# Optimization experiments

Measured on AMD Instinct MI355X. Metric: run time of the kernel, lower is better.

The kernel has to match this reference:

```python
import jax, jax.numpy as jnp
import numpy as np

H = 2048; HQ = 16; HKV = 4; G = HQ // HKV; D = 128; S = 2048
KS = 32; KSTRIDE = 16; BS = 128; TOPK = 8
INIT_BLK = 1; LOCAL_BLK = 2; WIN = 512
THETA = 500000.0
N_CMP = (S - KS) // KSTRIDE + 1
N_BLK = S // BS
NEG = -1e30


def _rope_inv_freq():
    # llama3-style frequency scaling (factor 8, high 4, low 1, orig 8192)
    inv = 1.0 / (THETA ** (np.arange(0, D, 2, dtype=np.float64) / D))
    factor, lo_f, hi_f, orig = 8.0, 1.0, 4.0, 8192.0
    wav = 2.0 * np.pi / inv
    smooth = (orig / wav - lo_f) / (hi_f - lo_f)
    inv_s = np.where(wav > orig / lo_f, inv / factor,
                     np.where(wav < orig / hi_f, inv,
                              (1.0 - smooth) * inv / factor + smooth * inv))
    return jnp.asarray(inv_s, dtype=jnp.float32)


def _rope(x):
    # x: [S, h, D]
    ang = jnp.arange(x.shape[0], dtype=jnp.float32)[:, None] * _rope_inv_freq()[None, :]
    cos = jnp.cos(ang)[:, None, :]
    sin = jnp.sin(ang)[:, None, :]
    x1, x2 = x[..., : D // 2], x[..., D // 2:]
    return jnp.concatenate([x1 * cos - x2 * sin, x2 * cos + x1 * sin], axis=-1)


def setup_inputs() -> dict:
    key = jax.random.key(0)
    ks = jax.random.split(key, 8)
    std = 0.02
    return {
        'hidden_states': jax.random.normal(ks[0], (1, S, H), jnp.float32),
        'Wq': jax.random.normal(ks[1], (H, HQ * D), jnp.float32) * std,
        'Wk': jax.random.normal(ks[2], (H, HKV * D), jnp.float32) * std,
        'Wv': jax.random.normal(ks[3], (H, HKV * D), jnp.float32) * std,
        'Wo': jax.random.normal(ks[4], (HQ * D, H), jnp.float32) * std,
        'Wg': jax.random.normal(ks[5], (H, HQ * 3), jnp.float32) * std,
        'Wck': jax.random.normal(ks[6], (HKV, KS * D, D), jnp.float32) * std,
        'Wcv': jax.random.normal(ks[7], (HKV, KS * D, D), jnp.float32) * std,
    }


def _nsa_forward(hidden_states, Wq, Wk, Wv, Wo, Wg, Wck, Wcv):
    x = hidden_states[0]                                  # [S, H] (bsz=1, packed)
    q = _rope((x @ Wq).reshape(S, HQ, D))                 # [S, HQ, D]
    k = _rope((x @ Wk).reshape(S, HKV, D))                # [S, HKV, D]
    v = (x @ Wv).reshape(S, HKV, D)
    scale = D ** -0.5
    pos = jnp.arange(S)
    qg = q.reshape(S, HKV, G, D)

    # ---- branch 1: compressed attention (overlapping windows, learned pooling) ----
    starts = jnp.arange(N_CMP) * KSTRIDE
    widx = starts[:, None] + jnp.arange(KS)[None, :]      # [N_CMP, KS]
    kw = k[widx].transpose(2, 0, 1, 3).reshape(HKV, N_CMP, KS * D)
    vw = v[widx].transpose(2, 0, 1, 3).reshape(HKV, N_CMP, KS * D)
    ck = jnp.einsum('hnf,hfd->hnd', kw, Wck)              # [HKV, N_CMP, D]
    cv = jnp.einsum('hnf,hfd->hnd', vw, Wcv)
    s_cmp = jnp.einsum('shgd,hnd->hgsn', qg, ck) * scale  # [HKV, G, S, N_CMP]
    m_cmp = (starts + KS)[None, :] <= pos[:, None] + 1    # fully-past compressed blocks
    has_cmp = m_cmp.any(axis=-1).astype(s_cmp.dtype)      # [S]
    p_cmp = jax.nn.softmax(jnp.where(m_cmp[None, None], s_cmp, NEG), axis=-1)
    p_cmp = p_cmp * has_cmp[None, None, :, None]
    o_cmp = jnp.einsum('hgsn,hnd->shgd', p_cmp, cv).reshape(S, HQ, D)

    # ---- branch 2: top-k block-selected attention ----
    cmp2blk = (starts // BS)[:, None] == jnp.arange(N_BLK)[None, :]
    bscore = jnp.einsum('hgsn,nb->hsb', p_cmp, cmp2blk.astype(p_cmp.dtype))  # GQA-group sum
    qblk = pos // BS
    blks = jnp.arange(N_BLK)
    forced = (blks[None, :] < INIT_BLK) | ((blks[None, :] <= qblk[:, None]) & (blks[None, :] > qblk[:, None] - LOCAL_BLK))
    _, top_idx = jax.lax.top_k(bscore + forced[None].astype(bscore.dtype) * 1e9, TOPK)
    sel_blk = jnp.any(top_idx[..., None] == blks, axis=-2)  # [HKV, S, N_BLK]

    causal = pos[None, :] <= pos[:, None]                    # [S, S]
    raw = jnp.einsum('shgd,nhd->hgsn', qg, k) * scale        # [HKV, G, S, S] (shared by branches 2/3)

    m_sel = jnp.repeat(sel_blk, BS, axis=-1) & causal[None]  # [HKV, S, S]
    p_sel = jax.nn.softmax(jnp.where(m_sel[:, None], raw, NEG), axis=-1)
    o_sel = jnp.einsum('hgsn,nhd->shgd', p_sel, v).reshape(S, HQ, D)

    # ---- branch 3: sliding-window attention ----
    m_win = causal & (pos[None, :] > pos[:, None] - WIN)
    p_win = jax.nn.softmax(jnp.where(m_win[None, None], raw, NEG), axis=-1)
    o_win = jnp.einsum('hgsn,nhd->shgd', p_win, v).reshape(S, HQ, D)

    # ---- per-head sigmoid gates mixing the three branches ----
    g = jax.nn.sigmoid(x @ Wg).reshape(S, HQ, 3)
    o = g[..., 0:1] * o_cmp + g[..., 1:2] * o_sel + g[..., 2:3] * o_win
    return (o.reshape(S, HQ * D) @ Wo)[None]                 # [1, S, H]


def reference(hidden_states, Wq, Wk, Wv, Wo, Wg, Wck, Wcv):
    return _nsa_forward(hidden_states, Wq, Wk, Wv, Wo, Wg, Wck, Wcv)
```

## Files before the change

kernel.cpp:

```cpp
#include <hip/hip_runtime.h>
#include <math.h>

#define SS 2048
#define HH 2048
#define HQ 16
#define HKV 4
#define GG 4
#define DD 128
#define KS 32
#define KSTRIDE 16
#define NCMP 127
#define NBLK 16
#define TOPK 8
#define WINSZ 512
#define TQ 16

typedef unsigned short u16;
typedef __bf16 bf16x8 __attribute__((ext_vector_type(8)));
typedef __bf16 bf16x4 __attribute__((ext_vector_type(4)));
typedef float f32x4 __attribute__((ext_vector_type(4)));

__device__ __forceinline__ u16 f2bf(float f) {
    __bf16 b = (__bf16)f;
    return __builtin_bit_cast(u16, b);
}

__device__ __forceinline__ int xcd_swz(int id, int nwg) {
    if (nwg & 7) return id;
    int cpx = nwg >> 3;
    return (id & 7) * cpx + (id >> 3);
}

__global__ void rope_tab(float* __restrict__ cost, float* __restrict__ sint) {
    int s = blockIdx.x;
    int i = threadIdx.x;
    double inv = pow(500000.0, -(double)i / 64.0);
    double wav = 6.283185307179586476925286766559 / inv;
    double inv_s;
    if (wav > 8192.0) inv_s = inv / 8.0;
    else if (wav < 2048.0) inv_s = inv;
    else {
        double sm = (8192.0 / wav - 1.0) / 3.0;
        inv_s = (1.0 - sm) * inv / 8.0 + sm * inv;
    }
    float ang = (float)s * (float)inv_s;
    cost[s * 64 + i] = cosf(ang);
    sint[s * 64 + i] = sinf(ang);
}

__global__ void rope_bf16(const float* __restrict__ src, u16* __restrict__ dst,
                          const float* __restrict__ cost, const float* __restrict__ sint,
                          int nh, float scale) {
    int s = blockIdx.x, h = blockIdx.y, i = threadIdx.x;
    const float* p = src + ((size_t)s * nh + h) * DD;
    float c = cost[s * 64 + i], sn = sint[s * 64 + i];
    float x1 = p[i], x2 = p[i + 64];
    u16* d = dst + ((size_t)s * nh + h) * DD;
    d[i] = f2bf((x1 * c - x2 * sn) * scale);
    d[i + 64] = f2bf((x2 * c + x1 * sn) * scale);
}

__global__ void sigmoid_k(float* __restrict__ x, int n) {
    int i = blockIdx.x * 256 + threadIdx.x;
    if (i < n) x[i] = 1.f / (1.f + __expf(-x[i]));
}

__global__ void conv_bf16(const float* __restrict__ in, u16* __restrict__ out, int n4) {
    int i = blockIdx.x * 256 + threadIdx.x;
    if (i < n4) {
        float4 v = ((const float4*)in)[i];
        ushort4 o;
        o.x = f2bf(v.x); o.y = f2bf(v.y); o.z = f2bf(v.z); o.w = f2bf(v.w);
        ((ushort4*)out)[i] = o;
    }
}

__global__ __launch_bounds__(256) void conv_vt(const float* __restrict__ v, u16* __restrict__ vt) {
    __shared__ float tile[32][33];
    int s0 = blockIdx.x * 32, d0 = blockIdx.y * 32, h = blockIdx.z;
    int tx = threadIdx.x & 31, ty = threadIdx.x >> 5;
#pragma unroll
    for (int i = 0; i < 32; i += 8)
        tile[ty + i][tx] = v[(size_t)(s0 + ty + i) * (HKV * DD) + h * DD + d0 + tx];
    __syncthreads();
#pragma unroll
    for (int i = 0; i < 32; i += 8)
        vt[(size_t)h * DD * SS + (size_t)(d0 + ty + i) * SS + s0 + tx] = f2bf(tile[tx][ty + i]);
}

__global__ __launch_bounds__(256) void convT(const float* __restrict__ W, u16* __restrict__ Bt,
                                             int K, int N, int Npad,
                                             size_t wz, size_t bz) {
    __shared__ float tile[32][33];
    W += (size_t)blockIdx.z * wz;
    Bt += (size_t)blockIdx.z * bz;
    int bk = blockIdx.x * 32, bn = blockIdx.y * 32;
    int tx = threadIdx.x & 31, ty = threadIdx.x >> 5;
#pragma unroll
    for (int i = 0; i < 32; i += 8) {
        int k = bk + ty + i, n = bn + tx;
        tile[ty + i][tx] = (n < N) ? W[(size_t)k * N + n] : 0.f;
    }
    __syncthreads();
#pragma unroll
    for (int i = 0; i < 32; i += 8) {
        int n = bn + ty + i, k = bk + tx;
        if (n < Npad) Bt[(size_t)n * K + k] = f2bf(tile[tx][ty + i]);
    }
}

__device__ __forceinline__ void gload16(const void* g, void* l) {
    __builtin_amdgcn_global_load_lds((const __attribute__((address_space(1))) void*)g,
                                     (__attribute__((address_space(3))) void*)l, 16, 0, 0);
}

__global__ __launch_bounds__(256) void gemm_mfma(const u16* __restrict__ A,
                                                 const u16* __restrict__ Bt,
                                                 float* __restrict__ C,
                                                 int M, int N, int K) {
    __shared__ __align__(16) u16 Asm[128 * 64];
    __shared__ __align__(16) u16 Bsm[128 * 64];
    int t = threadIdx.x;
    int lane = t & 63;
    int w = t >> 6;
    int wm = w >> 1, wn = w & 1;
    int nwg = gridDim.x * gridDim.y;
    int id = xcd_swz(blockIdx.y * gridDim.x + blockIdx.x, nwg);
    int bxs = id % gridDim.x, bys = id / gridDim.x;
    int bm = bys * 128, bn = bxs * 128;
    int lr = lane & 15, hi = lane >> 4;

    f32x4 acc[4][4] = {};
    for (int k0 = 0; k0 < K; k0 += 64) {
        if (k0) __syncthreads();
#pragma unroll
        for (int i = 0; i < 4; ++i) {
            int cflat = i * 256 + t;
            int m = cflat >> 3;
            int g = cflat & 7;
            int gl = g ^ (m & 7);
            unsigned lofs = (unsigned)((i * 256 + (t & ~63)) * 16);
            gload16(A + (size_t)(bm + m) * K + k0 + gl * 8, (char*)Asm + lofs);
            gload16(Bt + (size_t)(bn + m) * K + k0 + gl * 8, (char*)Bsm + lofs);
        }
        __syncthreads();
#pragma unroll
        for (int kk = 0; kk < 2; ++kk) {
            bf16x8 af[4], bf[4];
#pragma unroll
            for (int mi = 0; mi < 4; ++mi) {
                int row = wm * 64 + mi * 16 + lr;
                int g = (kk * 4 + hi) ^ (row & 7);
                af[mi] = *reinterpret_cast<const bf16x8*>(&Asm[row * 64 + g * 8]);
            }
#pragma unroll
            for (int ni = 0; ni < 4; ++ni) {
                int row = wn * 64 + ni * 16 + lr;
                int g = (kk * 4 + hi) ^ (row & 7);
                bf[ni] = *reinterpret_cast<const bf16x8*>(&Bsm[row * 64 + g * 8]);
            }
#pragma unroll
            for (int mi = 0; mi < 4; ++mi)
#pragma unroll
                for (int ni = 0; ni < 4; ++ni)
                    acc[mi][ni] = __builtin_amdgcn_mfma_f32_16x16x32_bf16(af[mi], bf[ni], acc[mi][ni], 0, 0, 0);
        }
    }
#pragma unroll
    for (int mi = 0; mi < 4; ++mi) {
#pragma unroll
        for (int ni = 0; ni < 4; ++ni) {
            int col = bn + wn * 64 + ni * 16 + lr;
            if (col < N) {
#pragma unroll
                for (int r = 0; r < 4; ++r) {
                    int row = bm + wm * 64 + mi * 16 + hi * 4 + r;
                    C[(size_t)row * N + col] = acc[mi][ni][r];
                }
            }
        }
    }
}

__global__ __launch_bounds__(256) void gemm_proj(const u16* __restrict__ A,
                                                 const u16* __restrict__ BtQ,
                                                 const u16* __restrict__ BtK,
                                                 const u16* __restrict__ BtV,
                                                 const u16* __restrict__ BtG,
                                                 float* __restrict__ Cq,
                                                 float* __restrict__ Ck,
                                                 float* __restrict__ Cv,
                                                 float* __restrict__ Cg) {
    __shared__ __align__(16) u16 Asm[128 * 64];
    __shared__ __align__(16) u16 Bsm[128 * 64];
    int nwg = gridDim.x * gridDim.y;
    int id = xcd_swz(blockIdx.y * gridDim.x + blockIdx.x, nwg);
    int bx = id % gridDim.x, by = id / gridDim.x;
    const u16* Bt; float* C; int N; int bn;
    if (bx < 16)      { Bt = BtQ; C = Cq; N = 2048; bn = bx * 128; }
    else if (bx < 20) { Bt = BtK; C = Ck; N = 512;  bn = (bx - 16) * 128; }
    else if (bx < 24) { Bt = BtV; C = Cv; N = 512;  bn = (bx - 20) * 128; }
    else              { Bt = BtG; C = Cg; N = 48;   bn = 0; }
    const int K = 2048;
    int t = threadIdx.x, lane = t & 63, w = t >> 6;
    int wm = w >> 1, wn = w & 1;
    int bm = by * 128;
    int lr = lane & 15, hi = lane >> 4;

    f32x4 acc[4][4] = {};
    for (int k0 = 0; k0 < K; k0 += 64) {
        if (k0) __syncthreads();
#pragma unroll
        for (int i = 0; i < 4; ++i) {
            int cflat = i * 256 + t;
            int m = cflat >> 3;
            int g = cflat & 7;
            int gl = g ^ (m & 7);
            unsigned lofs = (unsigned)((i * 256 + (t & ~63)) * 16);
            gload16(A + (size_t)(bm + m) * K + k0 + gl * 8, (char*)Asm + lofs);
            gload16(Bt + (size_t)(bn + m) * K + k0 + gl * 8, (char*)Bsm + lofs);
        }
        __syncthreads();
#pragma unroll
        for (int kk = 0; kk < 2; ++kk) {
            bf16x8 af[4], bf[4];
#pragma unroll
            for (int mi = 0; mi < 4; ++mi) {
                int row = wm * 64 + mi * 16 + lr;
                int g = (kk * 4 + hi) ^ (row & 7);
                af[mi] = *reinterpret_cast<const bf16x8*>(&Asm[row * 64 + g * 8]);
            }
#pragma unroll
            for (int ni = 0; ni < 4; ++ni) {
                int row = wn * 64 + ni * 16 + lr;
                int g = (kk * 4 + hi) ^ (row & 7);
                bf[ni] = *reinterpret_cast<const bf16x8*>(&Bsm[row * 64 + g * 8]);
            }
#pragma unroll
            for (int mi = 0; mi < 4; ++mi)
#pragma unroll
                for (int ni = 0; ni < 4; ++ni)
                    acc[mi][ni] = __builtin_amdgcn_mfma_f32_16x16x32_bf16(af[mi], bf[ni], acc[mi][ni], 0, 0, 0);
        }
    }
#pragma unroll
    for (int mi = 0; mi < 4; ++mi) {
#pragma unroll
        for (int ni = 0; ni < 4; ++ni) {
            int col = bn + wn * 64 + ni * 16 + lr;
            if (col < N) {
#pragma unroll
                for (int r = 0; r < 4; ++r) {
                    int row = bm + wm * 64 + mi * 16 + hi * 4 + r;
                    C[(size_t)row * N + col] = acc[mi][ni][r];
                }
            }
        }
    }
}

__global__ __launch_bounds__(256) void cmp_kv_split(const u16* __restrict__ Ak,
                                                    const u16* __restrict__ Wkt,
                                                    const u16* __restrict__ Av,
                                                    const u16* __restrict__ Wvt,
                                                    float* __restrict__ partials) {
    __shared__ __align__(16) u16 Asm[128 * 64];
    __shared__ __align__(16) u16 Bsm[128 * 64];
    int z = blockIdx.y, split = blockIdx.x;
    int h = z & 3;
    const u16* A  = (z >> 2) ? Av : Ak;
    const u16* Wt = (z >> 2) ? Wvt : Wkt;
    int t = threadIdx.x, lane = t & 63, w = t >> 6;
    int wm = w >> 1, wn = w & 1;
    int lr = lane & 15, hi = lane >> 4;
    const u16* Wh = Wt + (size_t)h * DD * (KS * DD);

    f32x4 acc[4][4] = {};
    int kbase = split * 256;
    for (int it = 0; it < 4; ++it) {
        int k0 = kbase + it * 64;
        if (it) __syncthreads();
        int roff = k0 >> 7;
        int dbase = ((k0 >> 6) & 1) * 64;
#pragma unroll
        for (int i = 0; i < 4; ++i) {
            int cflat = i * 256 + t;
            int m = cflat >> 3;
            int g = cflat & 7;
            int gl = g ^ (m & 7);
            unsigned lofs = (unsigned)((i * 256 + (t & ~63)) * 16);
            int nr = (m < NCMP) ? m : (NCMP - 1);
            gload16(A + ((size_t)(nr * KSTRIDE + roff) * HKV + h) * DD + dbase + gl * 8,
                    (char*)Asm + lofs);
            gload16(Wh + (size_t)m * (KS * DD) + k0 + gl * 8, (char*)Bsm + lofs);
        }
        __syncthreads();
#pragma unroll
        for (int kk = 0; kk < 2; ++kk) {
            bf16x8 af[4], bf[4];
#pragma unroll
            for (int mi = 0; mi < 4; ++mi) {
                int row = wm * 64 + mi * 16 + lr;
                int g = (kk * 4 + hi) ^ (row & 7);
                af[mi] = *reinterpret_cast<const bf16x8*>(&Asm[row * 64 + g * 8]);
            }
#pragma unroll
            for (int ni = 0; ni < 4; ++ni) {
                int row = wn * 64 + ni * 16 + lr;
                int g = (kk * 4 + hi) ^ (row & 7);
                bf[ni] = *reinterpret_cast<const bf16x8*>(&Bsm[row * 64 + g * 8]);
            }
#pragma unroll
            for (int mi = 0; mi < 4; ++mi)
#pragma unroll
                for (int ni = 0; ni < 4; ++ni)
                    acc[mi][ni] = __builtin_amdgcn_mfma_f32_16x16x32_bf16(af[mi], bf[ni], acc[mi][ni], 0, 0, 0);
        }
    }
    float* Cout = partials + ((size_t)(z * 16 + split)) * 128 * 128;
#pragma unroll
    for (int mi = 0; mi < 4; ++mi)
#pragma unroll
        for (int ni = 0; ni < 4; ++ni) {
            int col = wn * 64 + ni * 16 + lr;
#pragma unroll
            for (int r = 0; r < 4; ++r) {
                int row = wm * 64 + mi * 16 + hi * 4 + r;
                Cout[(size_t)row * 128 + col] = acc[mi][ni][r];
            }
        }
}

__global__ void cmp_kv_reduce(const float* __restrict__ partials,
                              u16* __restrict__ ckbf, u16* __restrict__ cvtbf) {
    int row = blockIdx.x, z = blockIdx.y, col = threadIdx.x;
    float s = 0.f;
#pragma unroll
    for (int sp = 0; sp < 16; ++sp)
        s += partials[(((size_t)z * 16 + sp) * 128 + row) * 128 + col];
    if (z < 4) ckbf[((size_t)z * 128 + row) * 128 + col] = f2bf(s);
    else       cvtbf[((size_t)(z - 4) * 128 + col) * 128 + row] = f2bf(s);
}

__global__ __launch_bounds__(256) void cmp_attn_mfma(
    const u16* __restrict__ qbf,
    const u16* __restrict__ ckbf,
    const u16* __restrict__ cvtbf,
    const float* __restrict__ gate,
    float* __restrict__ o_acc,
    unsigned int* __restrict__ sel) {
    __shared__ __align__(16) u16 Cks[128 * 128];
    __shared__ __align__(16) u16 P2[4][16 * 128];
    __shared__ float bs[4][16][16];
    int t = threadIdx.x, lane = t & 63, w = t >> 6;
    int lr = lane & 15, hi = lane >> 4;
    int s0 = blockIdx.x * 16, h = blockIdx.y;
    int hq = h * GG + w;
    int sr = s0 + lr;
    const u16* ckh = ckbf + (size_t)h * 128 * 128;
    const u16* cvh = cvtbf + (size_t)h * 128 * 128;
    bf16x8 qf[4];
#pragma unroll
    for (int ks = 0; ks < 4; ++ks)
        qf[ks] = *reinterpret_cast<const bf16x8*>(
            &qbf[((size_t)sr * HQ + hq) * DD + ks * 32 + hi * 8]);
#pragma unroll
    for (int i = 0; i < 8; ++i) {
        int id = i * 256 + t;
        int key = id >> 4, sub = id & 15;
        gload16(ckh + (size_t)key * 128 + ((sub ^ (key & 7)) * 8),
                (char*)Cks + (id & ~63) * 16);
    }
    __syncthreads();
    f32x4 sacc[8] = {};
#pragma unroll
    for (int ks = 0; ks < 4; ++ks)
#pragma unroll
        for (int mt = 0; mt < 8; ++mt) {
            int row = mt * 16 + lr;
            bf16x8 kf = *reinterpret_cast<const bf16x8*>(
                &Cks[row * 128 + (((ks * 4 + hi) ^ (row & 7)) * 8)]);
            sacc[mt] = __builtin_amdgcn_mfma_f32_16x16x32_bf16(kf, qf[ks], sacc[mt], 0, 0, 0);
        }
    int nv = (sr >= 31) ? ((sr - 31) >> 4) + 1 : 0;
    float e[8][4];
    float mx = -1e30f;
#pragma unroll
    for (int mt = 0; mt < 8; ++mt)
#pragma unroll
        for (int r = 0; r < 4; ++r) {
            int n = mt * 16 + hi * 4 + r;
            float x = (n < nv) ? sacc[mt][r] : -1e30f;
            e[mt][r] = x;
            mx = fmaxf(mx, x);
        }
    mx = fmaxf(mx, __shfl_xor(mx, 16, 64));
    mx = fmaxf(mx, __shfl_xor(mx, 32, 64));
    float l = 0.f;
#pragma unroll
    for (int mt = 0; mt < 8; ++mt)
#pragma unroll
        for (int r = 0; r < 4; ++r) {
            int n = mt * 16 + hi * 4 + r;
            float p = (n < nv) ? __expf(e[mt][r] - mx) : 0.f;
            e[mt][r] = p;
            l += p;
        }
    l += __shfl_xor(l, 16, 64);
    l += __shfl_xor(l, 32, 64);
    float invl = (nv > 0) ? 1.f / l : 0.f;
#pragma unroll
    for (int mt = 0; mt < 8; ++mt)
#pragma unroll
        for (int r = 0; r < 4; ++r) e[mt][r] *= invl;
#pragma unroll
    for (int mt = 0; mt < 8; ++mt) {
        bf16x4 pk;
        pk[0] = (__bf16)e[mt][0]; pk[1] = (__bf16)e[mt][1];
        pk[2] = (__bf16)e[mt][2]; pk[3] = (__bf16)e[mt][3];
        int grp = mt * 2 + (hi >> 1);
        int idx = lr * 128 + ((grp ^ (lr & 7)) * 8) + (hi & 1) * 4;
        *reinterpret_cast<bf16x4*>(&P2[w][idx]) = pk;
    }
#pragma unroll
    for (int mt = 0; mt < 8; ++mt) {
        float s4 = e[mt][0] + e[mt][1] + e[mt][2] + e[mt][3];
        float v = s4 + __shfl_xor(s4, 16, 64);
        if (hi == 0) bs[w][lr][mt * 2] = v;
        else if (hi == 2) bs[w][lr][mt * 2 + 1] = v;
    }
    __syncthreads();
    bf16x8 pa[4];
#pragma unroll
    for (int kslot = 0; kslot < 4; ++kslot)
        pa[kslot] = *reinterpret_cast<const bf16x8*>(
            &P2[w][lr * 128 + (((kslot * 4 + hi) ^ (lr & 7)) * 8)]);
    f32x4 Os[8] = {};
#pragma unroll
    for (int nt = 0; nt < 8; ++nt) {
        int d = nt * 16 + lr;
#pragma unroll
        for (int kslot = 0; kslot < 4; ++kslot) {
            bf16x8 bv = *reinterpret_cast<const bf16x8*>(
                &cvh[(size_t)d * 128 + kslot * 32 + hi * 8]);
            Os[nt] = __builtin_amdgcn_mfma_f32_16x16x32_bf16(pa[kslot], bv, Os[nt], 0, 0, 0);
        }
    }
#pragma unroll
    for (int r = 0; r < 4; ++r) {
        int q = hi * 4 + r;
        int srow = s0 + q;
        float g0 = gate[((size_t)srow * HQ + hq) * 3 + 0];
#pragma unroll
        for (int nt = 0; nt < 8; ++nt) {
            size_t idx = ((size_t)srow * HQ + hq) * DD + nt * 16 + lr;
            o_acc[idx] = g0 * Os[nt][r];
        }
    }
    if (t < 16) {
        int q = t, s = s0 + q;
        int qblk = s >> 7;
#pragma unroll
        for (int b = 0; b < 16; ++b) {
            bool forced = (b == 0) || (b <= qblk && b > qblk - 2);
            bs[0][q][b] = bs[0][q][b] + bs[1][q][b] + bs[2][q][b] + bs[3][q][b]
                          + (forced ? 1e9f : 0.f);
        }
        unsigned int mask = 0;
        for (int it = 0; it < TOPK; ++it) {
            int arg = 0; float best = bs[0][q][0];
            for (int b = 1; b < 16; ++b) {
                float x = bs[0][q][b];
                if (x > best) { best = x; arg = b; }
            }
            mask |= 1u << arg;
            bs[0][q][arg] = -1e38f;
        }
        sel[s * HKV + h] = mask;
    }
}

__global__ __launch_bounds__(256, 3) void sel_win_mfma(
    const u16* __restrict__ qbf,
    const u16* __restrict__ kbf,
    const u16* __restrict__ vtbf,
    const float* __restrict__ gate,
    const unsigned int* __restrict__ sel,
    const float* __restrict__ oacc,
    u16* __restrict__ outb) {
    __shared__ __align__(16) u16 Ks[64 * 128];
    __shared__ __align__(16) u16 Vs[128 * 64];
    __shared__ __align__(16) u16 P2[4][2][16 * 64];
    __shared__ unsigned int sml[16];
    int t = threadIdx.x, lane = t & 63, w = t >> 6;
    int lr = lane & 15, hi = lane >> 4;
    int s0 = (gridDim.x - 1 - blockIdx.x) * 16;
    int h = blockIdx.y;
    int hq = h * GG + w;
    int sr = s0 + lr;
    if (t < 16) sml[t] = sel[(s0 + t) * HKV + h];
    bf16x8 qf[4];
#pragma unroll
    for (int ks = 0; ks < 4; ++ks)
        qf[ks] = *reinterpret_cast<const bf16x8*>(
            &qbf[((size_t)(s0 + lr) * HQ + hq) * DD + ks * 32 + hi * 8]);
    __syncthreads();
    unsigned mymask = sml[lr];
    unsigned orMask = 0;
#pragma unroll
    for (int i = 0; i < 16; ++i) orMask |= sml[i];
    float m_u = -1e30f, l_s = 0.f, l_w = 0.f;
    f32x4 Os[8] = {}, Ow[8] = {};
    int smax = s0 + 15;
    const u16* vbase = vtbf + (size_t)h * DD * SS;

    for (int kb = 0; kb * 128 <= smax; ++kb) {
        bool needSel = (orMask >> kb) & 1u;
        bool selbit = needSel && ((mymask >> kb) & 1u);
        for (int half = 0; half < 2; ++half) {
            int hst = kb * 128 + half * 64;
            if (hst > smax) break;
            bool hWin = (hst + 63 >= s0 - (WINSZ - 1));
            if (!(needSel || hWin)) continue;
            __syncthreads();
#pragma unroll
            for (int i = 0; i < 4; ++i) {
                int id = i * 256 + t;
                int key = id >> 4, dq = id & 15;
                gload16(kbf + ((size_t)(hst + key) * HKV + h) * DD + ((dq ^ (key & 7)) * 8),
                        (char*)Ks + (id & ~63) * 16);
                int d = id >> 3, kq = id & 7;
                gload16(vbase + (size_t)d * SS + hst + ((kq ^ (d & 7)) * 8),
                        (char*)Vs + (id & ~63) * 16);
            }
            __syncthreads();
            f32x4 sacc[4] = {};
            __builtin_amdgcn_s_setprio(1);
#pragma unroll
            for (int ks = 0; ks < 4; ++ks) {
#pragma unroll
                for (int mt = 0; mt < 4; ++mt) {
                    int key = mt * 16 + lr;
                    bf16x8 kf = *reinterpret_cast<const bf16x8*>(
                        &Ks[key * 128 + (((ks * 4 + hi) ^ (key & 7)) * 8)]);
                    sacc[mt] = __builtin_amdgcn_mfma_f32_16x16x32_bf16(kf, qf[ks], sacc[mt], 0, 0, 0);
                }
            }
            __builtin_amdgcn_s_setprio(0);
            float e4[4][4];
            float mx = -1e30f;
#pragma unroll
            for (int mt = 0; mt < 4; ++mt)
#pragma unroll
                for (int r = 0; r < 4; ++r) {
                    int key = hst + mt * 16 + hi * 4 + r;
                    bool vS = selbit && (key <= sr);
                    bool vW = hWin && (key <= sr) && (key > sr - WINSZ);
                    float e = (vS || vW) ? sacc[mt][r] : -1e30f;
                    e4[mt][r] = e;
                    mx = fmaxf(mx, e);
                }
            mx = fmaxf(mx, __shfl_xor(mx, 16, 64));
            mx = fmaxf(mx, __shfl_xor(mx, 32, 64));
            if (!__all(mx - m_u <= 8.f)) {
                float newm = fmaxf(m_u, mx);
                float corr = __expf(m_u - newm);
                m_u = newm;
                l_s *= corr; l_w *= corr;
#pragma unroll
                for (int r = 0; r < 4; ++r) {
                    float c2 = __shfl(corr, hi * 4 + r, 64);
#pragma unroll
                    for (int nt = 0; nt < 8; ++nt) { Os[nt][r] *= c2; Ow[nt][r] *= c2; }
                }
            }
            float lsA = 0.f, lwA = 0.f;
#pragma unroll
            for (int mt = 0; mt < 4; ++mt)
#pragma unroll
                for (int r = 0; r < 4; ++r) {
                    int key = hst + mt * 16 + hi * 4 + r;
                    bool vS = selbit && (key <= sr);
                    bool vW = hWin && (key <= sr) && (key > sr - WINSZ);
                    float e = (vS || vW) ? __expf(e4[mt][r] - m_u) : 0.f;
                    e4[mt][r] = e;
                    lsA += vS ? e : 0.f;
                    lwA += vW ? e : 0.f;
                }
            lsA += __shfl_xor(lsA, 16, 64); lsA += __shfl_xor(lsA, 32, 64);
            lwA += __shfl_xor(lwA, 16, 64); lwA += __shfl_xor(lwA, 32, 64);
            l_s += lsA; l_w += lwA;
            if (needSel) {
#pragma unroll
                for (int mt = 0; mt < 4; ++mt) {
                    bf16x4 pk;
#pragma unroll
                    for (int r = 0; r < 4; ++r) {
                        int key = hst + mt * 16 + hi * 4 + r;
                        bool vS = selbit && (key <= sr);
                        pk[r] = (__bf16)(vS ? e4[mt][r] : 0.f);
                    }
                    int grp = mt * 2 + (hi >> 1);
                    int idx = lr * 64 + ((grp ^ (lr & 7)) * 8) + (hi & 1) * 4;
                    *reinterpret_cast<bf16x4*>(&P2[w][0][idx]) = pk;
                }
            }
            if (hWin) {
#pragma unroll
                for (int mt = 0; mt < 4; ++mt) {
                    bf16x4 pk;
#pragma unroll
                    for (int r = 0; r < 4; ++r) {
                        int key = hst + mt * 16 + hi * 4 + r;
                        bool vW = (key <= sr) && (key > sr - WINSZ);
                        pk[r] = (__bf16)(vW ? e4[mt][r] : 0.f);
                    }
                    int grp = mt * 2 + (hi >> 1);
                    int idx = lr * 64 + ((grp ^ (lr & 7)) * 8) + (hi & 1) * 4;
                    *reinterpret_cast<bf16x4*>(&P2[w][1][idx]) = pk;
                }
            }
            bf16x8 pas0, pas1, paw0, paw1;
            if (needSel) {
                pas0 = *reinterpret_cast<const bf16x8*>(&P2[w][0][lr * 64 + (((0 + hi) ^ (lr & 7)) * 8)]);
                pas1 = *reinterpret_cast<const bf16x8*>(&P2[w][0][lr * 64 + (((4 + hi) ^ (lr & 7)) * 8)]);
            }
            if (hWin) {
                paw0 = *reinterpret_cast<const bf16x8*>(&P2[w][1][lr * 64 + (((0 + hi) ^ (lr & 7)) * 8)]);
                paw1 = *reinterpret_cast<const bf16x8*>(&P2[w][1][lr * 64 + (((4 + hi) ^ (lr & 7)) * 8)]);
            }
            __builtin_amdgcn_s_setprio(1);
#pragma unroll
            for (int nt = 0; nt < 8; ++nt) {
                int d = nt * 16 + lr;
                bf16x8 bv0 = *reinterpret_cast<const bf16x8*>(&Vs[d * 64 + (((0 + hi) ^ (d & 7)) * 8)]);
                bf16x8 bv1 = *reinterpret_cast<const bf16x8*>(&Vs[d * 64 + (((4 + hi) ^ (d & 7)) * 8)]);
                if (needSel) {
                    Os[nt] = __builtin_amdgcn_mfma_f32_16x16x32_bf16(pas0, bv0, Os[nt], 0, 0, 0);
                    Os[nt] = __builtin_amdgcn_mfma_f32_16x16x32_bf16(pas1, bv1, Os[nt], 0, 0, 0);
                }
                if (hWin) {
                    Ow[nt] = __builtin_amdgcn_mfma_f32_16x16x32_bf16(paw0, bv0, Ow[nt], 0, 0, 0);
                    Ow[nt] = __builtin_amdgcn_mfma_f32_16x16x32_bf16(paw1, bv1, Ow[nt], 0, 0, 0);
                }
            }
            __builtin_amdgcn_s_setprio(0);
        }
    }
    float invls = (l_s > 0.f) ? 1.f / l_s : 0.f;
    float invlw = (l_w > 0.f) ? 1.f / l_w : 0.f;
#pragma unroll
    for (int r = 0; r < 4; ++r) {
        int q = hi * 4 + r;
        int srow = s0 + q;
        float a1 = gate[((size_t)srow * HQ + hq) * 3 + 1] * __shfl(invls, q, 64);
        float a2 = gate[((size_t)srow * HQ + hq) * 3 + 2] * __shfl(invlw, q, 64);
#pragma unroll
        for (int nt = 0; nt < 8; ++nt) {
            size_t idx = ((size_t)srow * HQ + hq) * DD + nt * 16 + lr;
            outb[idx] = f2bf(oacc[idx] + a1 * Os[nt][r] + a2 * Ow[nt][r]);
        }
    }
}

extern "C" void kernel_launch(void* const* d_in, const int* in_sizes, int n_in,
                              void* d_out, int out_size, void* d_ws, size_t ws_size,
                              hipStream_t stream) {
    const float* x   = (const float*)d_in[0];
    const float* Wq  = (const float*)d_in[1];
    const float* Wk  = (const float*)d_in[2];
    const float* Wv  = (const float*)d_in[3];
    const float* Wo  = (const float*)d_in[4];
    const float* Wg  = (const float*)d_in[5];
    const float* Wck = (const float*)d_in[6];
    const float* Wcv = (const float*)d_in[7];
    float* out = (float*)d_out;
    char* w = (char*)d_ws;
    float* qb   = (float*)(w + 0);
    float* kb   = (float*)(w + 16777216);
    float* vb   = (float*)(w + 20971520);
    float* g3   = (float*)(w + 25165824);
    u16* ckbf   = (u16*)(w + 25559040);
    u16* cvtbf  = (u16*)(w + 25819136);
    unsigned int* selb = (unsigned int*)(w + 26079232);
    float* cost = (float*)(w + 26112000);
    float* sint = (float*)(w + 26636288);
    float* oacc = (float*)(w + 27160576);
    u16* xb     = (u16*)(w + 43937792);
    u16* oaccb  = (u16*)(w + 52326400);
    u16* Wq_t   = (u16*)(w + 60715008);
    u16* Wo_t   = (u16*)(w + 69103616);
    u16* Wk_t   = (u16*)(w + 77492224);
    u16* Wv_t   = (u16*)(w + 79589376);
    u16* Wg_t   = (u16*)(w + 81686528);
    u16* qbf = Wq_t;
    u16* kbf = Wk_t;
    u16* vtbf = Wv_t;
    u16* vbf = (u16*)kb;
    u16* Wck_t = oaccb;
    u16* Wcv_t = xb;
    float* partials = oacc;

    hipLaunchKernelGGL(rope_tab, dim3(SS), dim3(64), 0, stream, cost, sint);
    hipLaunchKernelGGL(conv_bf16, dim3(4096), dim3(256), 0, stream, x, xb, SS * HH / 4);
    hipLaunchKernelGGL(convT, dim3(64, 64), dim3(256), 0, stream, Wq, Wq_t, HH, 2048, 2048, 0, 0);
    hipLaunchKernelGGL(convT, dim3(64, 16), dim3(256), 0, stream, Wk, Wk_t, HH, 512, 512, 0, 0);
    hipLaunchKernelGGL(convT, dim3(64, 16), dim3(256), 0, stream, Wv, Wv_t, HH, 512, 512, 0, 0);
    hipLaunchKernelGGL(convT, dim3(64, 4),  dim3(256), 0, stream, Wg, Wg_t, HH, 48, 128, 0, 0);
    hipLaunchKernelGGL(convT, dim3(64, 64), dim3(256), 0, stream, Wo, Wo_t, HQ * DD, 2048, 2048, 0, 0);
    hipLaunchKernelGGL(gemm_proj, dim3(25, 16), dim3(256), 0, stream,
                       xb, Wq_t, Wk_t, Wv_t, Wg_t, qb, kb, vb, g3);
    hipLaunchKernelGGL(rope_bf16, dim3(SS, HQ),  dim3(64), 0, stream, qb, qbf, cost, sint, HQ, 0.08838834764831845f);
    hipLaunchKernelGGL(rope_bf16, dim3(SS, HKV), dim3(64), 0, stream, kb, kbf, cost, sint, HKV, 1.0f);
    hipLaunchKernelGGL(sigmoid_k, dim3((SS * HQ * 3 + 255) / 256), dim3(256), 0, stream, g3, SS * HQ * 3);
    hipLaunchKernelGGL(conv_bf16, dim3(1024), dim3(256), 0, stream, vb, vbf, SS * HKV * DD / 4);
    hipLaunchKernelGGL(conv_vt, dim3(64, 4, 4), dim3(256), 0, stream, vb, vtbf);
    hipLaunchKernelGGL(convT, dim3(128, 4, 4), dim3(256), 0, stream,
                       Wck, Wck_t, KS * DD, DD, DD, (size_t)KS * DD * DD, (size_t)DD * KS * DD);
    hipLaunchKernelGGL(convT, dim3(128, 4, 4), dim3(256), 0, stream,
                       Wcv, Wcv_t, KS * DD, DD, DD, (size_t)KS * DD * DD, (size_t)DD * KS * DD);
    hipLaunchKernelGGL(cmp_kv_split, dim3(16, 8), dim3(256), 0, stream,
                       kbf, Wck_t, vbf, Wcv_t, partials);
    hipLaunchKernelGGL(cmp_kv_reduce, dim3(128, 8), dim3(128), 0, stream,
                       partials, ckbf, cvtbf);
    hipLaunchKernelGGL(cmp_attn_mfma, dim3(SS / TQ, HKV), dim3(256), 0, stream,
                       qbf, ckbf, cvtbf, g3, oacc, selb);
    hipLaunchKernelGGL(sel_win_mfma, dim3(SS / TQ, HKV), dim3(256), 0, stream,
                       qbf, kbf, vtbf, g3, selb, oacc, oaccb);
    hipLaunchKernelGGL(gemm_mfma, dim3(16, 16), dim3(256), 0, stream, oaccb, Wo_t, out, 2048, 2048, 2048);
}
```

Baseline: 264.7 us.

## Prefetch next active K/V tile into registers while computing current tile

The sel/window attention loop now walks a flattened list of active 64-key tiles. It loads the next active tile's K and V into registers before computing on the current tile, instead of issuing direct global-to-LDS loads and waiting on them each iteration. This is meant to hide global load latency behind the MFMA and softmax work. In exchange it costs extra VGPRs for the staging registers, which may lower occupancy, and adds a register-to-LDS store step per tile.

```diff
diff --git a/kernel.cpp b/kernel.cpp
--- a/kernel.cpp
+++ b/kernel.cpp
@@ -514,138 +514,165 @@
     int smax = s0 + 15;
     const u16* vbase = vtbf + (size_t)h * DD * SS;
 
-    for (int kb = 0; kb * 128 <= smax; ++kb) {
-        bool needSel = (orMask >> kb) & 1u;
-        bool selbit = needSel && ((mymask >> kb) & 1u);
-        for (int half = 0; half < 2; ++half) {
-            int hst = kb * 128 + half * 64;
-            if (hst > smax) break;
-            bool hWin = (hst + 63 >= s0 - (WINSZ - 1));
-            if (!(needSel || hWin)) continue;
-            __syncthreads();
+    auto isActive = [&](int p) -> bool {
+        int kb = p >> 7;
+        bool ns = (orMask >> kb) & 1u;
+        bool hw = (p + 63 >= s0 - (WINSZ - 1));
+        return ns || hw;
+    };
+    bf16x8 kreg[4], vreg[4];
+    int hst = 0;
+    while (hst <= smax && !isActive(hst)) hst += 64;
+#pragma unroll
+    for (int i = 0; i < 4; ++i) {
+        int id = i * 256 + t;
+        int key = id >> 4, dq = id & 15;
+        kreg[i] = *reinterpret_cast<const bf16x8*>(
+            &kbf[((size_t)(hst + key) * HKV + h) * DD + ((dq ^ (key & 7)) * 8)]);
+        int d = id >> 3, kq = id & 7;
+        vreg[i] = *reinterpret_cast<const bf16x8*>(
+            &vbase[(size_t)d * SS + hst + ((kq ^ (d & 7)) * 8)]);
+    }
+
+    while (hst <= smax) {
+        int nxt = hst + 64;
+        while (nxt <= smax && !isActive(nxt)) nxt += 64;
+        __syncthreads();
+#pragma unroll
+        for (int i = 0; i < 4; ++i) {
+            int id = i * 256 + t;
+            *reinterpret_cast<bf16x8*>((char*)Ks + id * 16) = kreg[i];
+            *reinterpret_cast<bf16x8*>((char*)Vs + id * 16) = vreg[i];
+        }
+        __syncthreads();
+        if (nxt <= smax) {
 #pragma unroll
             for (int i = 0; i < 4; ++i) {
                 int id = i * 256 + t;
                 int key = id >> 4, dq = id & 15;
-                gload16(kbf + ((size_t)(hst + key) * HKV + h) * DD + ((dq ^ (key & 7)) * 8),
-                        (char*)Ks + (id & ~63) * 16);
+                kreg[i] = *reinterpret_cast<const bf16x8*>(
+                    &kbf[((size_t)(nxt + key) * HKV + h) * DD + ((dq ^ (key & 7)) * 8)]);
                 int d = id >> 3, kq = id & 7;
-                gload16(vbase + (size_t)d * SS + hst + ((kq ^ (d & 7)) * 8),
-                        (char*)Vs + (id & ~63) * 16);
-            }
-            __syncthreads();
-            f32x4 sacc[4] = {};
-            __builtin_amdgcn_s_setprio(1);
-#pragma unroll
-            for (int ks = 0; ks < 4; ++ks) {
-#pragma unroll
-                for (int mt = 0; mt < 4; ++mt) {
-                    int key = mt * 16 + lr;
-                    bf16x8 kf = *reinterpret_cast<const bf16x8*>(
-                        &Ks[key * 128 + (((ks * 4 + hi) ^ (key & 7)) * 8)]);
-                    sacc[mt] = __builtin_amdgcn_mfma_f32_16x16x32_bf16(kf, qf[ks], sacc[mt], 0, 0, 0);
-                }
-            }
-            __builtin_amdgcn_s_setprio(0);
-            float e4[4][4];
-            float mx = -1e30f;
-#pragma unroll
-            for (int mt = 0; mt < 4; ++mt)
+                vreg[i] = *reinterpret_cast<const bf16x8*>(
+                    &vbase[(size_t)d * SS + nxt + ((kq ^ (d & 7)) * 8)]);
+            }
+        }
+        int kb = hst >> 7;
+        bool needSel = (orMask >> kb) & 1u;
+        bool selbit = needSel && ((mymask >> kb) & 1u);
+        bool hWin = (hst + 63 >= s0 - (WINSZ - 1));
+        f32x4 sacc[4] = {};
+        __builtin_amdgcn_s_setprio(1);
+#pragma unroll
+        for (int ks = 0; ks < 4; ++ks) {
+#pragma unroll
+            for (int mt = 0; mt < 4; ++mt) {
+                int key = mt * 16 + lr;
+                bf16x8 kf = *reinterpret_cast<const bf16x8*>(
+                    &Ks[key * 128 + (((ks * 4 + hi) ^ (key & 7)) * 8)]);
+                sacc[mt] = __builtin_amdgcn_mfma_f32_16x16x32_bf16(kf, qf[ks], sacc[mt], 0, 0, 0);
+            }
+        }
+        __builtin_amdgcn_s_setprio(0);
+        float e4[4][4];
+        float mx = -1e30f;
+#pragma unroll
+        for (int mt = 0; mt < 4; ++mt)
+#pragma unroll
+            for (int r = 0; r < 4; ++r) {
+                int key = hst + mt * 16 + hi * 4 + r;
+                bool vS = selbit && (key <= sr);
+                bool vW = hWin && (key <= sr) && (key > sr - WINSZ);
+                float e = (vS || vW) ? sacc[mt][r] : -1e30f;
+                e4[mt][r] = e;
+                mx = fmaxf(mx, e);
+            }
+        mx = fmaxf(mx, __shfl_xor(mx, 16, 64));
+        mx = fmaxf(mx, __shfl_xor(mx, 32, 64));
+        if (!__all(mx - m_u <= 8.f)) {
+            float newm = fmaxf(m_u, mx);
+            float corr = __expf(m_u - newm);
+            m_u = newm;
+            l_s *= corr; l_w *= corr;
+#pragma unroll
+            for (int r = 0; r < 4; ++r) {
+                float c2 = __shfl(corr, hi * 4 + r, 64);
+#pragma unroll
+                for (int nt = 0; nt < 8; ++nt) { Os[nt][r] *= c2; Ow[nt][r] *= c2; }
+            }
+        }
+        float lsA = 0.f, lwA = 0.f;
+#pragma unroll
+        for (int mt = 0; mt < 4; ++mt)
+#pragma unroll
+            for (int r = 0; r < 4; ++r) {
+                int key = hst + mt * 16 + hi * 4 + r;
+                bool vS = selbit && (key <= sr);
+                bool vW = hWin && (key <= sr) && (key > sr - WINSZ);
+                float e = (vS || vW) ? __expf(e4[mt][r] - m_u) : 0.f;
+                e4[mt][r] = e;
+                lsA += vS ? e : 0.f;
+                lwA += vW ? e : 0.f;
+            }
+        lsA += __shfl_xor(lsA, 16, 64); lsA += __shfl_xor(lsA, 32, 64);
+        lwA += __shfl_xor(lwA, 16, 64); lwA += __shfl_xor(lwA, 32, 64);
+        l_s += lsA; l_w += lwA;
+        if (needSel) {
+#pragma unroll
+            for (int mt = 0; mt < 4; ++mt) {
+                bf16x4 pk;
 #pragma unroll
                 for (int r = 0; r < 4; ++r) {
                     int key = hst + mt * 16 + hi * 4 + r;
                     bool vS = selbit && (key <= sr);
-                    bool vW = hWin && (key <= sr) && (key > sr - WINSZ);
-                    float e = (vS || vW) ? sacc[mt][r] : -1e30f;
-                    e4[mt][r] = e;
-                    mx = fmaxf(mx, e);
+                    pk[r] = (__bf16)(vS ? e4[mt][r] : 0.f);
                 }
-            mx = fmaxf(mx, __shfl_xor(mx, 16, 64));
-            mx = fmaxf(mx, __shfl_xor(mx, 32, 64));
-            if (!__all(mx - m_u <= 8.f)) {
-                float newm = fmaxf(m_u, mx);
-                float corr = __expf(m_u - newm);
-                m_u = newm;
-                l_s *= corr; l_w *= corr;
-#pragma unroll
-                for (int r = 0; r < 4; ++r) {
-                    float c2 = __shfl(corr, hi * 4 + r, 64);
-#pragma unroll
-                    for (int nt = 0; nt < 8; ++nt) { Os[nt][r] *= c2; Ow[nt][r] *= c2; }
-                }
-            }
-            float lsA = 0.f, lwA = 0.f;
-#pragma unroll
-            for (int mt = 0; mt < 4; ++mt)
+                int grp = mt * 2 + (hi >> 1);
+                int idx = lr * 64 + ((grp ^ (lr & 7)) * 8) + (hi & 1) * 4;
+                *reinterpret_cast<bf16x4*>(&P2[w][0][idx]) = pk;
+            }
+        }
+        if (hWin) {
+#pragma unroll
+            for (int mt = 0; mt < 4; ++mt) {
+                bf16x4 pk;
 #pragma unroll
                 for (int r = 0; r < 4; ++r) {
                     int key = hst + mt * 16 + hi * 4 + r;
-                    bool vS = selbit && (key <= sr);
-                    bool vW = hWin && (key <= sr) && (key > sr - WINSZ);
-                    float e = (vS || vW) ? __expf(e4[mt][r] - m_u) : 0.f;
-                    e4[mt][r] = e;
-                    lsA += vS ? e : 0.f;
-                    lwA += vW ? e : 0.f;
+                    bool vW = (key <= sr) && (key > sr - WINSZ);
+                    pk[r] = (__bf16)(vW ? e4[mt][r] : 0.f);
                 }
-            lsA += __shfl_xor(lsA, 16, 64); lsA += __shfl_xor(lsA, 32, 64);
-            lwA += __shfl_xor(lwA, 16, 64); lwA += __shfl_xor(lwA, 32, 64);
-            l_s += lsA; l_w += lwA;
+                int grp = mt * 2 + (hi >> 1);
+                int idx = lr * 64 + ((grp ^ (lr & 7)) * 8) + (hi & 1) * 4;
+                *reinterpret_cast<bf16x4*>(&P2[w][1][idx]) = pk;
+            }
+        }
+        bf16x8 pas0, pas1, paw0, paw1;
+        if (needSel) {
+            pas0 = *reinterpret_cast<const bf16x8*>(&P2[w][0][lr * 64 + (((0 + hi) ^ (lr & 7)) * 8)]);
+            pas1 = *reinterpret_cast<const bf16x8*>(&P2[w][0][lr * 64 + (((4 + hi) ^ (lr & 7)) * 8)]);
+        }
+        if (hWin) {
+            paw0 = *reinterpret_cast<const bf16x8*>(&P2[w][1][lr * 64 + (((0 + hi) ^ (lr & 7)) * 8)]);
+            paw1 = *reinterpret_cast<const bf16x8*>(&P2[w][1][lr * 64 + (((4 + hi) ^ (lr & 7)) * 8)]);
+        }
+        __builtin_amdgcn_s_setprio(1);
+#pragma unroll
+        for (int nt = 0; nt < 8; ++nt) {
+            int d = nt * 16 + lr;
+            bf16x8 bv0 = *reinterpret_cast<const bf16x8*>(&Vs[d * 64 + (((0 + hi) ^ (d & 7)) * 8)]);
+            bf16x8 bv1 = *reinterpret_cast<const bf16x8*>(&Vs[d * 64 + (((4 + hi) ^ (d & 7)) * 8)]);
             if (needSel) {
-#pragma unroll
-                for (int mt = 0; mt < 4; ++mt) {
-                    bf16x4 pk;
-#pragma unroll
-                    for (int r = 0; r < 4; ++r) {
-                        int key = hst + mt * 16 + hi * 4 + r;
-                        bool vS = selbit && (key <= sr);
-                        pk[r] = (__bf16)(vS ? e4[mt][r] : 0.f);
-                    }
-                    int grp = mt * 2 + (hi >> 1);
-                    int idx = lr * 64 + ((grp ^ (lr & 7)) * 8) + (hi & 1) * 4;
-                    *reinterpret_cast<bf16x4*>(&P2[w][0][idx]) = pk;
-                }
+                Os[nt] = __builtin_amdgcn_mfma_f32_16x16x32_bf16(pas0, bv0, Os[nt], 0, 0, 0);
+                Os[nt] = __builtin_amdgcn_mfma_f32_16x16x32_bf16(pas1, bv1, Os[nt], 0, 0, 0);
             }
             if (hWin) {
-#pragma unroll
-                for (int mt = 0; mt < 4; ++mt) {
-                    bf16x4 pk;
-#pragma unroll
-                    for (int r = 0; r < 4; ++r) {
-                        int key = hst + mt * 16 + hi * 4 + r;
-                        bool vW = (key <= sr) && (key > sr - WINSZ);
-                        pk[r] = (__bf16)(vW ? e4[mt][r] : 0.f);
-                    }
-                    int grp = mt * 2 + (hi >> 1);
-                    int idx = lr * 64 + ((grp ^ (lr & 7)) * 8) + (hi & 1) * 4;
-                    *reinterpret_cast<bf16x4*>(&P2[w][1][idx]) = pk;
-                }
-            }
-            bf16x8 pas0, pas1, paw0, paw1;
-            if (needSel) {
-                pas0 = *reinterpret_cast<const bf16x8*>(&P2[w][0][lr * 64 + (((0 + hi) ^ (lr & 7)) * 8)]);
-                pas1 = *reinterpret_cast<const bf16x8*>(&P2[w][0][lr * 64 + (((4 + hi) ^ (lr & 7)) * 8)]);
-            }
-            if (hWin) {
-                paw0 = *reinterpret_cast<const bf16x8*>(&P2[w][1][lr * 64 + (((0 + hi) ^ (lr & 7)) * 8)]);
-                paw1 = *reinterpret_cast<const bf16x8*>(&P2[w][1][lr * 64 + (((4 + hi) ^ (lr & 7)) * 8)]);
-            }
-            __builtin_amdgcn_s_setprio(1);
-#pragma unroll
-            for (int nt = 0; nt < 8; ++nt) {
-                int d = nt * 16 + lr;
-                bf16x8 bv0 = *reinterpret_cast<const bf16x8*>(&Vs[d * 64 + (((0 + hi) ^ (d & 7)) * 8)]);
-                bf16x8 bv1 = *reinterpret_cast<const bf16x8*>(&Vs[d * 64 + (((4 + hi) ^ (d & 7)) * 8)]);
-                if (needSel) {
-                    Os[nt] = __builtin_amdgcn_mfma_f32_16x16x32_bf16(pas0, bv0, Os[nt], 0, 0, 0);
-                    Os[nt] = __builtin_amdgcn_mfma_f32_16x16x32_bf16(pas1, bv1, Os[nt], 0, 0, 0);
-                }
-                if (hWin) {
-                    Ow[nt] = __builtin_amdgcn_mfma_f32_16x16x32_bf16(paw0, bv0, Ow[nt], 0, 0, 0);
-                    Ow[nt] = __builtin_amdgcn_mfma_f32_16x16x32_bf16(paw1, bv1, Ow[nt], 0, 0, 0);
-                }
-            }
-            __builtin_amdgcn_s_setprio(0);
-        }
+                Ow[nt] = __builtin_amdgcn_mfma_f32_16x16x32_bf16(paw0, bv0, Ow[nt], 0, 0, 0);
+                Ow[nt] = __builtin_amdgcn_mfma_f32_16x16x32_bf16(paw1, bv1, Ow[nt], 0, 0, 0);
+            }
+        }
+        __builtin_amdgcn_s_setprio(0);
+        hst = nxt;
     }
     float invls = (l_s > 0.f) ? 1.f / l_s : 0.f;
     float invlw = (l_w > 0.f) ? 1.f / l_w : 0.f;
```

New measurement: 377.2 us. 42.5% more time.
